# Optimization experiments

Hardware: AMD Instinct MI355X
Metric: run time of the kernel (lower is better)

## Reference

```python
import jax, jax.numpy as jnp
import numpy as np
from jax import lax

VOCAB = 10000
HID = 512
BATCH = 128
SEQ = 64
SCALE = 0.1


def setup_inputs() -> dict:
    key = jax.random.key(0)
    ks = jax.random.split(key, 16)
    u = lambda k, shape: jax.random.uniform(k, shape, jnp.float32, -SCALE, SCALE)
    return {
        "features": jax.random.randint(ks[0], (BATCH, SEQ), 0, VOCAB, jnp.int32),
        "labels": jax.random.randint(ks[1], (BATCH, SEQ), 0, VOCAB, jnp.int32),
        "seq_lengths": jax.random.randint(ks[2], (BATCH,), 0, SEQ, jnp.int32),
        "seq_mask": jax.random.uniform(ks[3], (BATCH, SEQ), jnp.float32),
        "embedding": u(ks[4], (VOCAB, HID)),
        "W0x": u(ks[5], (HID, 4 * HID)),
        "W0h": u(ks[6], (HID, 4 * HID)),
        "b0": jnp.zeros((4 * HID,), jnp.float32),
        "W1x": u(ks[7], (HID, 4 * HID)),
        "W1h": u(ks[8], (HID, 4 * HID)),
        "b1": jnp.zeros((4 * HID,), jnp.float32),
        "softmax_w": u(ks[9], (HID, VOCAB)),
        "softmax_b": jnp.zeros((VOCAB,), jnp.float32),
    }


def _lstm_cell(h, c, xin, Wx, Wh, b, m):
    # forget_bias = 0.0 (as in LSTMBlockCell(forget_bias=0.0))
    g = xin @ Wx + h @ Wh + b            # [B, 4H]
    i, cg, f, o = jnp.split(g, 4, axis=-1)
    c_new = jax.nn.sigmoid(f) * c + jax.nn.sigmoid(i) * jnp.tanh(cg)
    h_new = jax.nn.sigmoid(o) * jnp.tanh(c_new)
    # sequence_length masking: freeze state, zero output past length
    return m * h_new + (1 - m) * h, m * c_new + (1 - m) * c, m * h_new


def reference(features, labels, seq_lengths, seq_mask, embedding,
              W0x, W0h, b0, W1x, W1h, b1, softmax_w, softmax_b):
    x = embedding[features]                       # [B, T, H]
    B, T, H = x.shape
    xs = jnp.swapaxes(x, 0, 1)                    # [T, B, H]
    act = (jnp.arange(T)[:, None] < seq_lengths[None, :]).astype(x.dtype)[..., None]  # [T,B,1]

    def step(carry, inp):
        h0, c0, h1, c1 = carry
        xt, m = inp
        h0, c0, o0 = _lstm_cell(h0, c0, xt, W0x, W0h, b0, m)
        h1, c1, o1 = _lstm_cell(h1, c1, o0, W1x, W1h, b1, m)
        return (h0, c0, h1, c1), o1

    init = tuple(jnp.zeros((B, H), x.dtype) for _ in range(4))
    _, outs = lax.scan(step, init, (xs, act))     # [T, B, H]
    out = jnp.swapaxes(outs, 0, 1)                # [B, T, H]

    logits = out @ softmax_w + softmax_b          # [B, T, V]
    logp = jax.nn.log_softmax(logits, axis=-1)
    xent = -jnp.take_along_axis(logp, labels[..., None], axis=-1)[..., 0]  # [B, T]
    # tf.contrib.seq2seq.sequence_loss(average_across_batch=True, average_across_timesteps=False)
    loss_t = jnp.sum(xent * seq_mask, axis=0) / (jnp.sum(seq_mask, axis=0) + 1e-12)  # [T]
    cost = jnp.mean(loss_t)
    return cost
```

## Files before the change

### kernel.cpp

```cpp
#include <hip/hip_runtime.h>
#include <hip/hip_bf16.h>

#define BB 128
#define TT 64
#define HH 512
#define VV 10000
#define VP 10048
#define NTILES 157
#define NCHUNK 16
#define TPC 10
#define NBLK 256

typedef __attribute__((ext_vector_type(8))) __bf16 bf16x8;
typedef __attribute__((ext_vector_type(4))) float f32x4;
typedef unsigned short ushort_t;

__device__ __forceinline__ ushort_t f2bf(float x) {
  union { float f; unsigned u; } v; v.f = x;
  unsigned r = v.u + 0x7fffu + ((v.u >> 16) & 1u);
  return (ushort_t)(r >> 16);
}

__device__ __forceinline__ f32x4 mfma16(bf16x8 a, bf16x8 b, f32x4 c) {
  return __builtin_amdgcn_mfma_f32_16x16x32_bf16(a, b, c, 0, 0, 0);
}

__device__ __forceinline__ bf16x8 load16_sc1(const ushort_t* p) {
  bf16x8 r;
  asm volatile("global_load_dwordx4 %0, %1, off sc1" : "=v"(r) : "v"(p) : "memory");
  return r;
}

__device__ __forceinline__ void store16B_sc1(ushort_t* p, bf16x8 v) {
  asm volatile("global_store_dwordx4 %0, %1, off sc1" :: "v"(p), "v"(v) : "memory");
}

__device__ __forceinline__ void group_barrier(unsigned* bar, unsigned target, int grp) {
  asm volatile("s_waitcnt vmcnt(0)" ::: "memory");
  __syncthreads();
  if (threadIdx.x == 0) {
    const unsigned old = __hip_atomic_fetch_add(&bar[grp * 16], 1u,
                                                __ATOMIC_RELAXED, __HIP_MEMORY_SCOPE_AGENT);
    if (old + 1 == 64u * target)
      __hip_atomic_store(&bar[256 + grp * 16], target, __ATOMIC_RELAXED,
                         __HIP_MEMORY_SCOPE_AGENT);
    while (__hip_atomic_load(&bar[256 + grp * 16], __ATOMIC_RELAXED,
                             __HIP_MEMORY_SCOPE_AGENT) < target)
      __builtin_amdgcn_s_sleep(1);
  }
  __syncthreads();
}

__global__ void k_trans_w(const float* __restrict__ Wx0, const float* __restrict__ Wh0,
                          const float* __restrict__ Wx1, const float* __restrict__ Wh1,
                          ushort_t* __restrict__ dst0, ushort_t* __restrict__ dst1) {
  __shared__ float tile[64][65];
  const int kt = blockIdx.x * 64;
  const int ct = blockIdx.y * 64;
  const float* Wx = blockIdx.z ? Wx1 : Wx0;
  const float* Wh = blockIdx.z ? Wh1 : Wh0;
  ushort_t* dst = blockIdx.z ? dst1 : dst0;
  const int tid = threadIdx.x;
  const int cl = tid & 63;
  const int cp = ct + cl;
  const int col = (cp & 3) * 512 + (cp >> 2);
#pragma unroll
  for (int r = 0; r < 16; ++r) {
    const int kl = r * 4 + (tid >> 6);
    const int k = kt + kl;
    tile[cl][kl] = (k < 512) ? Wx[k * 2048 + col] : Wh[(k - 512) * 2048 + col];
  }
  __syncthreads();
#pragma unroll
  for (int s = 0; s < 16; ++s) {
    const int idx = tid + s * 256;
    const int cl2 = idx >> 6, kl2 = idx & 63;
    dst[(size_t)(ct + cl2) * 1024 + kt + kl2] = f2bf(tile[cl2][kl2]);
  }
}

__global__ void k_trans_sw(const float* __restrict__ sw, ushort_t* __restrict__ dst) {
  __shared__ float tile[64][65];
  const int kt = blockIdx.x * 64;
  const int vt = blockIdx.y * 64;
  const int tid = threadIdx.x;
  const int vl = tid & 63;
  const int v = vt + vl;
#pragma unroll
  for (int r = 0; r < 16; ++r) {
    const int kl = r * 4 + (tid >> 6);
    tile[vl][kl] = (v < VV) ? sw[(size_t)(kt + kl) * VV + v] : 0.f;
  }
  __syncthreads();
#pragma unroll
  for (int s = 0; s < 16; ++s) {
    const int idx = tid + s * 256;
    const int vl2 = idx >> 6, kl2 = idx & 63;
    dst[(size_t)(vt + vl2) * 512 + kt + kl2] = f2bf(tile[vl2][kl2]);
  }
}

__global__ void k_misc(const int* __restrict__ feat, const float* __restrict__ emb,
                       ushort_t* __restrict__ xb, ushort_t* __restrict__ h0,
                       ushort_t* __restrict__ h1, unsigned* __restrict__ bar) {
  const int stride = gridDim.x * blockDim.x;
  for (int e = blockIdx.x * blockDim.x + threadIdx.x; e < 8192 * 512; e += stride) {
    const int row = e >> 9;
    const int t = row >> 7, b = row & 127;
    const int f = feat[b * 64 + t];
    xb[e] = f2bf(emb[(size_t)f * 512 + (e & 511)]);
    if (e < 2 * 128 * 512) { h0[e] = 0; h1[e] = 0; }
    if (e < 512) bar[e] = 0u;
  }
}

__global__ __launch_bounds__(256, 1) void k_scan(
    const ushort_t* __restrict__ xb, const ushort_t* __restrict__ W0t,
    const ushort_t* __restrict__ W1t, const float* __restrict__ b0,
    const float* __restrict__ b1, ushort_t* __restrict__ h0g,
    ushort_t* __restrict__ h1g, ushort_t* __restrict__ out1,
    const int* __restrict__ seqlen, unsigned* __restrict__ bar) {
  __shared__ ushort_t act[32 * 128 * 8];
  __shared__ ushort_t hst[32][16];
  __shared__ ushort_t ost[32][16];
  __shared__ int sl_sh[32];
  const int bid = blockIdx.x;
  const int layer = bid >> 7;
  const int lb = bid & 127;
  const int cblk = lb >> 2;
  const int bquad = lb & 3;
  const int grp = bid & 3;
  const int tid = threadIdx.x;
  const int w = tid >> 6;
  const int lane = tid & 63;
  const int fr = lane & 15;
  const int hi = lane >> 4;
  const int w4hi = w * 4 + hi;

  const ushort_t* Wt = layer ? W1t : W0t;
  const float* bias = layer ? b1 : b0;
  ushort_t* hbuf = layer ? h1g : h0g;

  if (tid < 32) sl_sh[tid] = seqlen[bquad * 32 + tid];

  bf16x8 wreg[32];
  {
    const ushort_t* wp = Wt + (size_t)(cblk * 64 + w * 16 + fr) * 1024 + hi * 8;
#pragma unroll
    for (int ks = 0; ks < 32; ++ks)
      wreg[ks] = *reinterpret_cast<const bf16x8*>(wp + ks * 32);
  }

  const int u = cblk * 16 + w4hi;
  const float bi = bias[u];
  const float bc = bias[512 + u];
  const float bf_ = bias[1024 + u];
  const float bo = bias[1536 + u];

  __syncthreads();
  const int sl0 = sl_sh[fr];
  const int sl1 = sl_sh[fr + 16];

  float c0s = 0.f, c1s = 0.f;
  float h0s = 0.f, h1s = 0.f;

#pragma unroll 1
  for (int p = 0; p <= 64; ++p) {
    const int t = layer ? (p - 1) : p;
    const bool active = layer ? (p >= 1) : (p < 64);

    if (layer == 0 && active) {
      const ushort_t* xsrc = xb + (size_t)t * 128 * 512;
#pragma unroll
      for (int i = 0; i < 8; ++i) {
        const int idx = i * 256 + tid;
        const int b = idx >> 6;
        const int kp = idx & 63;
        const int kslot = (kp & 0x30) | ((kp & 15) ^ (b & 15));
        const ushort_t* s = xsrc + (size_t)(bquad * 32 + b) * 512 + (kslot << 3);
        *reinterpret_cast<bf16x8*>(&act[(b * 128 + kp) * 8]) =
            *reinterpret_cast<const bf16x8*>(s);
      }
    }

    group_barrier(bar, (unsigned)(p + 1), grp);

    if (active) {
      if (layer == 1) {
        bf16x8 tmp[16];
        const ushort_t* xsrc = h0g + (size_t)(p & 1) * 128 * 512;
        const ushort_t* hsrc = h1g + (size_t)(t & 1) * 128 * 512;
        int dsts[16];
#pragma unroll
        for (int i = 0; i < 8; ++i) {
          const int idx = i * 256 + tid;
          const int b = idx >> 6;
          const int kp = idx & 63;
          const int kslot = (kp & 0x30) | ((kp & 15) ^ (b & 15));
          tmp[i] = load16_sc1(xsrc + (size_t)(bquad * 32 + b) * 512 + (kslot << 3));
          dsts[i] = (b * 128 + kp) * 8;
        }
#pragma unroll
        for (int i = 0; i < 8; ++i) {
          const int idx = i * 256 + tid;
          const int b = idx >> 6;
          const int kp = 64 + (idx & 63);
          const int kslot = (kp & 0x70) | ((kp & 15) ^ (b & 15));
          tmp[8 + i] = load16_sc1(hsrc + (size_t)(bquad * 32 + b) * 512 + ((kslot - 64) << 3));
          dsts[8 + i] = (b * 128 + kp) * 8;
        }
        asm volatile("s_waitcnt vmcnt(0)" ::: "memory");
        __builtin_amdgcn_sched_barrier(0);
        const bf16x8 ZV = {};
#pragma unroll
        for (int i = 0; i < 8; ++i) {
          const int b = (i * 256 + tid) >> 6;
          *reinterpret_cast<bf16x8*>(&act[dsts[i]]) = (t < sl_sh[b]) ? tmp[i] : ZV;
        }
#pragma unroll
        for (int i = 0; i < 8; ++i)
          *reinterpret_cast<bf16x8*>(&act[dsts[8 + i]]) = tmp[8 + i];
      } else {
        bf16x8 tmp[8];
        const ushort_t* hsrc = h0g + (size_t)(t & 1) * 128 * 512;
        int dsts[8];
#pragma unroll
        for (int i = 0; i < 8; ++i) {
          const int idx = i * 256 + tid;
          const int b = idx >> 6;
          const int kp = 64 + (idx & 63);
          const int kslot = (kp & 0x70) | ((kp & 15) ^ (b & 15));
          tmp[i] = load16_sc1(hsrc + (size_t)(bquad * 32 + b) * 512 + ((kslot - 64) << 3));
          dsts[i] = (b * 128 + kp) * 8;
        }
        asm volatile("s_waitcnt vmcnt(0)" ::: "memory");
        __builtin_amdgcn_sched_barrier(0);
#pragma unroll
        for (int i = 0; i < 8; ++i)
          *reinterpret_cast<bf16x8*>(&act[dsts[i]]) = tmp[i];
      }
      __syncthreads();

      f32x4 acc0 = (f32x4){0.f, 0.f, 0.f, 0.f};
      f32x4 acc1 = (f32x4){0.f, 0.f, 0.f, 0.f};
#pragma unroll
      for (int ks = 0; ks < 32; ++ks) {
        const int kslot = ks * 4 + hi;
        const int kp = (kslot & 0x70) | ((kslot & 15) ^ fr);
        const bf16x8 bf0 = *reinterpret_cast<const bf16x8*>(&act[(fr * 128 + kp) * 8]);
        const bf16x8 bf1 = *reinterpret_cast<const bf16x8*>(&act[((16 + fr) * 128 + kp) * 8]);
        acc0 = mfma16(wreg[ks], bf0, acc0);
        acc1 = mfma16(wreg[ks], bf1, acc1);
      }
      __syncthreads();

      {
        const float si = 1.f / (1.f + __expf(-(acc0[0] + bi)));
        const float tc = tanhf(acc0[1] + bc);
        const float sf = 1.f / (1.f + __expf(-(acc0[2] + bf_)));
        const float so = 1.f / (1.f + __expf(-(acc0[3] + bo)));
        const float cn = sf * c0s + si * tc;
        const float hn = so * tanhf(cn);
        const bool msk = t < sl0;
        if (msk) { c0s = cn; h0s = hn; }
        hst[fr][w4hi] = f2bf(h0s);
        if (layer) ost[fr][w4hi] = msk ? f2bf(hn) : (ushort_t)0;
      }
      {
        const float si = 1.f / (1.f + __expf(-(acc1[0] + bi)));
        const float tc = tanhf(acc1[1] + bc);
        const float sf = 1.f / (1.f + __expf(-(acc1[2] + bf_)));
        const float so = 1.f / (1.f + __expf(-(acc1[3] + bo)));
        const float cn = sf * c1s + si * tc;
        const float hn = so * tanhf(cn);
        const bool msk = t < sl1;
        if (msk) { c1s = cn; h1s = hn; }
        hst[fr + 16][w4hi] = f2bf(h1s);
        if (layer) ost[fr + 16][w4hi] = msk ? f2bf(hn) : (ushort_t)0;
      }
      __syncthreads();

      if (tid < 64) {
        const int bl = tid >> 1, hf = tid & 1;
        const size_t off = (size_t)(bquad * 32 + bl) * 512 + cblk * 16 + hf * 8;
        ushort_t* hp = hbuf + (size_t)((t + 1) & 1) * 128 * 512 + off;
        const bf16x8 hv = *reinterpret_cast<const bf16x8*>(&hst[bl][hf * 8]);
        store16B_sc1(hp, hv);
        if (layer) {
          const bf16x8 ovv = *reinterpret_cast<const bf16x8*>(&ost[bl][hf * 8]);
          *reinterpret_cast<bf16x8*>(out1 + (size_t)t * 128 * 512 + off) = ovv;
        }
      }
    }
  }
}

__global__ __launch_bounds__(256, 2) void k_loss_gemm(
    const ushort_t* __restrict__ A, const ushort_t* __restrict__ SWT,
    const float* __restrict__ sb, const int* __restrict__ labels,
    float* __restrict__ part) {
  __shared__ ushort_t Bl[64 * 512];
  const int tid = threadIdx.x;
  const int lane = tid & 63;
  const int w = tid >> 6;
  const int fr = lane & 15;
  const int fk = (lane >> 4) << 3;
  const int rowbase = blockIdx.x * 128 + w * 32;
  const int chunk = blockIdx.y;
  const int tile_lo = chunk * TPC;
  const int tile_hi = (tile_lo + TPC < NTILES) ? (tile_lo + TPC) : NTILES;

  bf16x8 a[2][16];
#pragma unroll
  for (int rf = 0; rf < 2; ++rf) {
    const ushort_t* ap = A + (size_t)(rowbase + rf * 16 + fr) * 512 + fk;
#pragma unroll
    for (int ks = 0; ks < 16; ++ks) a[rf][ks] = *reinterpret_cast<const bf16x8*>(ap + ks * 32);
  }

  int lab[2][4];
  float m[2][4], l[2][4], ll[2][4];
#pragma unroll
  for (int rf = 0; rf < 2; ++rf)
#pragma unroll
    for (int r = 0; r < 4; ++r) {
      const int rg = rowbase + rf * 16 + ((lane >> 4) << 2) + r;
      lab[rf][r] = labels[(rg & 127) * 64 + (rg >> 7)];
      m[rf][r] = -3.0e38f; l[rf][r] = 0.f; ll[rf][r] = 0.f;
    }

  for (int tile = tile_lo; tile < tile_hi; ++tile) {
    const ushort_t* bsrc = SWT + (size_t)tile * 64 * 512;
    __syncthreads();
#pragma unroll
    for (int s = 0; s < 16; ++s) {
      const int h = (s * 256 + tid) << 3;
      const int v = h >> 9;
      const int kb = (h & 511) >> 3;
      *reinterpret_cast<bf16x8*>(&Bl[v * 512 + ((kb ^ (v & 7)) << 3)]) =
          *reinterpret_cast<const bf16x8*>(bsrc + h);
    }
    __syncthreads();

    f32x4 acc[2][4];
#pragma unroll
    for (int rf = 0; rf < 2; ++rf)
#pragma unroll
      for (int cf = 0; cf < 4; ++cf) acc[rf][cf] = (f32x4){0.f, 0.f, 0.f, 0.f};

#pragma unroll
    for (int ks = 0; ks < 16; ++ks) {
#pragma unroll
      for (int cf = 0; cf < 4; ++cf) {
        const int v = cf * 16 + fr;
        const int kb = (ks * 32 + fk) >> 3;
        const bf16x8 b =
            *reinterpret_cast<const bf16x8*>(&Bl[v * 512 + ((kb ^ (v & 7)) << 3)]);
        acc[0][cf] = mfma16(a[0][ks], b, acc[0][cf]);
        acc[1][cf] = mfma16(a[1][ks], b, acc[1][cf]);
      }
    }

    const int vb = tile * 64;
    float sbt[4]; bool vld[4];
#pragma unroll
    for (int cf = 0; cf < 4; ++cf) {
      const int v = vb + cf * 16 + fr;
      vld[cf] = v < VV;
      sbt[cf] = vld[cf] ? sb[v] : 0.f;
    }
#pragma unroll
    for (int rf = 0; rf < 2; ++rf)
#pragma unroll
      for (int r = 0; r < 4; ++r) {
        const float x0 = vld[0] ? acc[rf][0][r] + sbt[0] : -3.0e38f;
        const float x1 = vld[1] ? acc[rf][1][r] + sbt[1] : -3.0e38f;
        const float x2 = vld[2] ? acc[rf][2][r] + sbt[2] : -3.0e38f;
        const float x3 = vld[3] ? acc[rf][3][r] + sbt[3] : -3.0e38f;
        const float tm = fmaxf(fmaxf(x0, x1), fmaxf(x2, x3));
        if (tm > -1.0e37f) {
          const float mn = fmaxf(m[rf][r], tm);
          const float sc = __expf(m[rf][r] - mn);
          const float se = __expf(x0 - mn) + __expf(x1 - mn) +
                           __expf(x2 - mn) + __expf(x3 - mn);
          l[rf][r] = l[rf][r] * sc + se;
          m[rf][r] = mn;
        }
        const int lt = lab[rf][r] - vb;
        if (lt >= 0 && lt < 64 && fr == (lt & 15)) {
          const int cf = lt >> 4;
          ll[rf][r] += (cf == 0) ? x0 : (cf == 1) ? x1 : (cf == 2) ? x2 : x3;
        }
      }
  }

#pragma unroll
  for (int rf = 0; rf < 2; ++rf)
#pragma unroll
    for (int r = 0; r < 4; ++r) {
      float mm = m[rf][r], lv = l[rf][r], lv2 = ll[rf][r];
#pragma unroll
      for (int sh = 1; sh < 16; sh <<= 1) {
        const float m2 = __shfl_xor(mm, sh, 64);
        const float l2 = __shfl_xor(lv, sh, 64);
        const float ll2 = __shfl_xor(lv2, sh, 64);
        const float mn = fmaxf(mm, m2);
        lv = lv * __expf(mm - mn) + l2 * __expf(m2 - mn);
        mm = mn;
        lv2 += ll2;
      }
      if (fr == 0) {
        const int rg = rowbase + rf * 16 + ((lane >> 4) << 2) + r;
        float* p = part + ((size_t)chunk * 8192 + rg) * 4;
        p[0] = mm; p[1] = lv; p[2] = lv2;
      }
    }
}

__global__ void k_loss_merge(const float* __restrict__ part, float* __restrict__ xent) {
  const int row = blockIdx.x * 256 + threadIdx.x;
  float m = -3.0e38f, l = 0.f, ll = 0.f;
#pragma unroll
  for (int c = 0; c < NCHUNK; ++c) {
    const float* p = part + ((size_t)c * 8192 + row) * 4;
    const float pm = p[0], pl = p[1], pll = p[2];
    const float mn = fmaxf(m, pm);
    l = l * __expf(m - mn) + pl * __expf(pm - mn);
    m = mn;
    ll += pll;
  }
  xent[row] = m + logf(l) - ll;
}

__global__ void k_final(const float* __restrict__ xent, const float* __restrict__ mask,
                        float* __restrict__ out) {
  __shared__ float partial[4];
  const int lane = threadIdx.x & 63;
  const int w = threadIdx.x >> 6;
  float accT = 0.f;
  for (int i = 0; i < 16; ++i) {
    const int t = w * 16 + i;
    const float m1 = mask[lane * 64 + t];
    const float m2 = mask[(lane + 64) * 64 + t];
    float s = xent[t * 128 + lane] * m1 + xent[t * 128 + lane + 64] * m2;
    float sm = m1 + m2;
#pragma unroll
    for (int sh = 1; sh < 64; sh <<= 1) {
      s += __shfl_xor(s, sh, 64);
      sm += __shfl_xor(sm, sh, 64);
    }
    accT += s / (sm + 1e-12f);
  }
  if (lane == 0) partial[w] = accT;
  __syncthreads();
  if (threadIdx.x == 0)
    out[0] = (partial[0] + partial[1] + partial[2] + partial[3]) * (1.f / 64.f);
}

extern "C" void kernel_launch(void* const* d_in, const int* in_sizes, int n_in,
                              void* d_out, int out_size, void* d_ws, size_t ws_size,
                              hipStream_t stream) {
  const int* feat = (const int*)d_in[0];
  const int* labels = (const int*)d_in[1];
  const int* seqlen = (const int*)d_in[2];
  const float* seqmask = (const float*)d_in[3];
  const float* emb = (const float*)d_in[4];
  const float* W0x = (const float*)d_in[5];
  const float* W0h = (const float*)d_in[6];
  const float* b0 = (const float*)d_in[7];
  const float* W1x = (const float*)d_in[8];
  const float* W1h = (const float*)d_in[9];
  const float* b1 = (const float*)d_in[10];
  const float* sw = (const float*)d_in[11];
  const float* sbv = (const float*)d_in[12];

  ushort_t* W0t = (ushort_t*)d_ws;
  ushort_t* W1t = W0t + (size_t)2048 * 1024;
  ushort_t* SWT = W1t + (size_t)2048 * 1024;
  ushort_t* xb = SWT + (size_t)VP * 512;
  ushort_t* out1 = xb + (size_t)8192 * 512;
  ushort_t* h0g = out1 + (size_t)8192 * 512;
  ushort_t* h1g = h0g + (size_t)2 * 128 * 512;
  float* xent = (float*)(h1g + (size_t)2 * 128 * 512);
  float* part = xent + 8192;
  unsigned* bar = (unsigned*)(part + (size_t)NCHUNK * 8192 * 4);

  k_trans_w<<<dim3(16, 32, 2), 256, 0, stream>>>(W0x, W0h, W1x, W1h, W0t, W1t);
  k_trans_sw<<<dim3(8, 157), 256, 0, stream>>>(sw, SWT);
  k_misc<<<4096, 256, 0, stream>>>(feat, emb, xb, h0g, h1g, bar);

  {
    const ushort_t* a0 = xb; const ushort_t* a1 = W0t; const ushort_t* a2 = W1t;
    const float* a3 = b0; const float* a4 = b1;
    ushort_t* a5 = h0g; ushort_t* a6 = h1g; ushort_t* a7 = out1;
    const int* a8 = seqlen; unsigned* a9 = bar;
    void* args[] = {(void*)&a0, (void*)&a1, (void*)&a2, (void*)&a3, (void*)&a4,
                    (void*)&a5, (void*)&a6, (void*)&a7, (void*)&a8, (void*)&a9};
    hipLaunchCooperativeKernel((const void*)k_scan, dim3(NBLK), dim3(256), args, 0, stream);
  }

  k_loss_gemm<<<dim3(64, NCHUNK), 256, 0, stream>>>(out1, SWT, sbv, labels, part);
  k_loss_merge<<<32, 256, 0, stream>>>(part, xent);
  k_final<<<1, 256, 0, stream>>>(xent, seqmask, (float*)d_out);
}
```

Measured before the change: 547.1 us.

## Double-buffer loss GEMM with direct global-to-LDS loads, split scan barrier, fast gates

The loss GEMM now stages half-tiles of the pre-swizzled softmax weights straight into double-buffered LDS with global_load_lds. The next half-tile loads while the current one is computed, and the softmax bias is cached in shared memory. The softmax-weight transpose kernel writes the XOR-swizzled layout directly, so the staging copy needs no per-element remap. In the scan, the group barrier is split so the arrive happens before the layer-0 input prefetch and the wait after it, and sigmoid/tanh use exp plus a hardware reciprocal. This targets load latency in the loss GEMM and barrier idle time in the scan, at some cost in activation precision.

```diff
diff --git a/kernel.cpp b/kernel.cpp
--- a/kernel.cpp
+++ b/kernel.cpp
@@ -25,6 +25,13 @@
   return __builtin_amdgcn_mfma_f32_16x16x32_bf16(a, b, c, 0, 0, 0);
 }
 
+__device__ __forceinline__ float fsig(float x) {
+  return __builtin_amdgcn_rcpf(1.f + __expf(-x));
+}
+__device__ __forceinline__ float ftanh(float x) {
+  return 1.f - 2.f * __builtin_amdgcn_rcpf(__expf(2.f * x) + 1.f);
+}
+
 __device__ __forceinline__ bf16x8 load16_sc1(const ushort_t* p) {
   bf16x8 r;
   asm volatile("global_load_dwordx4 %0, %1, off sc1" : "=v"(r) : "v"(p) : "memory");
@@ -35,20 +42,10 @@
   asm volatile("global_store_dwordx4 %0, %1, off sc1" :: "v"(p), "v"(v) : "memory");
 }
 
-__device__ __forceinline__ void group_barrier(unsigned* bar, unsigned target, int grp) {
-  asm volatile("s_waitcnt vmcnt(0)" ::: "memory");
-  __syncthreads();
-  if (threadIdx.x == 0) {
-    const unsigned old = __hip_atomic_fetch_add(&bar[grp * 16], 1u,
-                                                __ATOMIC_RELAXED, __HIP_MEMORY_SCOPE_AGENT);
-    if (old + 1 == 64u * target)
-      __hip_atomic_store(&bar[256 + grp * 16], target, __ATOMIC_RELAXED,
-                         __HIP_MEMORY_SCOPE_AGENT);
-    while (__hip_atomic_load(&bar[256 + grp * 16], __ATOMIC_RELAXED,
-                             __HIP_MEMORY_SCOPE_AGENT) < target)
-      __builtin_amdgcn_s_sleep(1);
-  }
-  __syncthreads();
+__device__ __forceinline__ void glds16(const ushort_t* g, ushort_t* l) {
+  __builtin_amdgcn_global_load_lds(
+      (const __attribute__((address_space(1))) unsigned*)g,
+      (__attribute__((address_space(3))) unsigned*)l, 16, 0, 0);
 }
 
 __global__ void k_trans_w(const float* __restrict__ Wx0, const float* __restrict__ Wh0,
@@ -96,7 +93,10 @@
   for (int s = 0; s < 16; ++s) {
     const int idx = tid + s * 256;
     const int vl2 = idx >> 6, kl2 = idx & 63;
-    dst[(size_t)(vt + vl2) * 512 + kt + kl2] = f2bf(tile[vl2][kl2]);
+    const int k = kt + kl2;
+    const int kb = k >> 3;
+    const int kp = (((kb ^ (vl2 & 7)) << 3) | (k & 7));
+    dst[(size_t)(vt + vl2) * 512 + kp] = f2bf(tile[vl2][kl2]);
   }
 }
 
@@ -169,6 +169,15 @@
     const int t = layer ? (p - 1) : p;
     const bool active = layer ? (p >= 1) : (p < 64);
 
+    asm volatile("s_waitcnt vmcnt(0)" ::: "memory");
+    __syncthreads();
+    if (tid == 0) {
+      const unsigned old = __hip_atomic_fetch_add(&bar[grp * 16], 1u,
+                                                  __ATOMIC_RELAXED, __HIP_MEMORY_SCOPE_AGENT);
+      if (old + 1 == 64u * (unsigned)(p + 1))
+        __hip_atomic_store(&bar[256 + grp * 16], (unsigned)(p + 1), __ATOMIC_RELAXED,
+                           __HIP_MEMORY_SCOPE_AGENT);
+    }
     if (layer == 0 && active) {
       const ushort_t* xsrc = xb + (size_t)t * 128 * 512;
 #pragma unroll
@@ -182,8 +191,12 @@
             *reinterpret_cast<const bf16x8*>(s);
       }
     }
-
-    group_barrier(bar, (unsigned)(p + 1), grp);
+    if (tid == 0) {
+      while (__hip_atomic_load(&bar[256 + grp * 16], __ATOMIC_RELAXED,
+                               __HIP_MEMORY_SCOPE_AGENT) < (unsigned)(p + 1))
+        __builtin_amdgcn_s_sleep(1);
+    }
+    __syncthreads();
 
     if (active) {
       if (layer == 1) {
@@ -255,24 +268,24 @@
       __syncthreads();
 
       {
-        const float si = 1.f / (1.f + __expf(-(acc0[0] + bi)));
-        const float tc = tanhf(acc0[1] + bc);
-        const float sf = 1.f / (1.f + __expf(-(acc0[2] + bf_)));
-        const float so = 1.f / (1.f + __expf(-(acc0[3] + bo)));
+        const float si = fsig(acc0[0] + bi);
+        const float tc = ftanh(acc0[1] + bc);
+        const float sf = fsig(acc0[2] + bf_);
+        const float so = fsig(acc0[3] + bo);
         const float cn = sf * c0s + si * tc;
-        const float hn = so * tanhf(cn);
+        const float hn = so * ftanh(cn);
         const bool msk = t < sl0;
         if (msk) { c0s = cn; h0s = hn; }
         hst[fr][w4hi] = f2bf(h0s);
         if (layer) ost[fr][w4hi] = msk ? f2bf(hn) : (ushort_t)0;
       }
       {
-        const float si = 1.f / (1.f + __expf(-(acc1[0] + bi)));
-        const float tc = tanhf(acc1[1] + bc);
-        const float sf = 1.f / (1.f + __expf(-(acc1[2] + bf_)));
-        const float so = 1.f / (1.f + __expf(-(acc1[3] + bo)));
+        const float si = fsig(acc1[0] + bi);
+        const float tc = ftanh(acc1[1] + bc);
+        const float sf = fsig(acc1[2] + bf_);
+        const float so = fsig(acc1[3] + bo);
         const float cn = sf * c1s + si * tc;
-        const float hn = so * tanhf(cn);
+        const float hn = so * ftanh(cn);
         const bool msk = t < sl1;
         if (msk) { c1s = cn; h1s = hn; }
         hst[fr + 16][w4hi] = f2bf(h1s);
@@ -296,10 +309,11 @@
 }
 
 __global__ __launch_bounds__(256, 2) void k_loss_gemm(
-    const ushort_t* __restrict__ A, const ushort_t* __restrict__ SWT,
+    const ushort_t* __restrict__ A, const ushort_t* __restrict__ SWTs,
     const float* __restrict__ sb, const int* __restrict__ labels,
     float* __restrict__ part) {
-  __shared__ ushort_t Bl[64 * 512];
+  __shared__ ushort_t Bl[2][32 * 512];
+  __shared__ float sbl[640];
   const int tid = threadIdx.x;
   const int lane = tid & 63;
   const int w = tid >> 6;
@@ -309,6 +323,12 @@
   const int chunk = blockIdx.y;
   const int tile_lo = chunk * TPC;
   const int tile_hi = (tile_lo + TPC < NTILES) ? (tile_lo + TPC) : NTILES;
+  const int nhalf = (tile_hi - tile_lo) * 2;
+
+  for (int i = tid; i < 640; i += 256) {
+    const int v = chunk * 640 + i;
+    sbl[i] = (v < VV) ? sb[v] : 0.f;
+  }
 
   bf16x8 a[2][16];
 #pragma unroll
@@ -328,71 +348,100 @@
       lab[rf][r] = labels[(rg & 127) * 64 + (rg >> 7)];
       m[rf][r] = -3.0e38f; l[rf][r] = 0.f; ll[rf][r] = 0.f;
     }
-
-  for (int tile = tile_lo; tile < tile_hi; ++tile) {
-    const ushort_t* bsrc = SWT + (size_t)tile * 64 * 512;
-    __syncthreads();
-#pragma unroll
-    for (int s = 0; s < 16; ++s) {
-      const int h = (s * 256 + tid) << 3;
-      const int v = h >> 9;
-      const int kb = (h & 511) >> 3;
-      *reinterpret_cast<bf16x8*>(&Bl[v * 512 + ((kb ^ (v & 7)) << 3)]) =
-          *reinterpret_cast<const bf16x8*>(bsrc + h);
-    }
-    __syncthreads();
-
-    f32x4 acc[2][4];
-#pragma unroll
-    for (int rf = 0; rf < 2; ++rf)
-#pragma unroll
-      for (int cf = 0; cf < 4; ++cf) acc[rf][cf] = (f32x4){0.f, 0.f, 0.f, 0.f};
-
-#pragma unroll
-    for (int ks = 0; ks < 16; ++ks) {
+  __syncthreads();
+
+#define STAGE(BUF, HIDX)                                                         \
+  do {                                                                           \
+    const size_t gbase = (size_t)(tile_lo * 2 + (HIDX)) * 32 * 512;              \
+    _Pragma("unroll")                                                            \
+    for (int i_ = 0; i_ < 8; ++i_) {                                             \
+      glds16(SWTs + gbase + (size_t)(i_ * 256 + tid) * 8,                        \
+             &Bl[BUF][i_ * 2048 + w * 512]);                                     \
+    }                                                                            \
+  } while (0)
+
+  f32x4 acc[2][4];
+  STAGE(0, 0);
+
+#pragma unroll 1
+  for (int idx = 0; idx < nhalf; ++idx) {
+    const int cur = idx & 1;
+    if (idx + 1 < nhalf) {
+      STAGE(cur ^ 1, idx + 1);
+      asm volatile("s_waitcnt vmcnt(8)" ::: "memory");
+    } else {
+      asm volatile("s_waitcnt vmcnt(0)" ::: "memory");
+    }
+    __builtin_amdgcn_s_barrier();
+    __builtin_amdgcn_sched_barrier(0);
+
+    if ((idx & 1) == 0) {
+      acc[0][0] = (f32x4){0.f,0.f,0.f,0.f}; acc[0][1] = (f32x4){0.f,0.f,0.f,0.f};
+      acc[1][0] = (f32x4){0.f,0.f,0.f,0.f}; acc[1][1] = (f32x4){0.f,0.f,0.f,0.f};
+#pragma unroll
+      for (int ks = 0; ks < 16; ++ks) {
+#pragma unroll
+        for (int j = 0; j < 2; ++j) {
+          const int vloc = j * 16 + fr;
+          const int kb = ks * 4 + (fk >> 3);
+          const bf16x8 b = *reinterpret_cast<const bf16x8*>(
+              &Bl[cur][vloc * 512 + ((kb ^ (vloc & 7)) << 3)]);
+          acc[0][j] = mfma16(a[0][ks], b, acc[0][j]);
+          acc[1][j] = mfma16(a[1][ks], b, acc[1][j]);
+        }
+      }
+    } else {
+      acc[0][2] = (f32x4){0.f,0.f,0.f,0.f}; acc[0][3] = (f32x4){0.f,0.f,0.f,0.f};
+      acc[1][2] = (f32x4){0.f,0.f,0.f,0.f}; acc[1][3] = (f32x4){0.f,0.f,0.f,0.f};
+#pragma unroll
+      for (int ks = 0; ks < 16; ++ks) {
+#pragma unroll
+        for (int j = 0; j < 2; ++j) {
+          const int vloc = j * 16 + fr;
+          const int kb = ks * 4 + (fk >> 3);
+          const bf16x8 b = *reinterpret_cast<const bf16x8*>(
+              &Bl[cur][vloc * 512 + ((kb ^ (vloc & 7)) << 3)]);
+          acc[0][2 + j] = mfma16(a[0][ks], b, acc[0][2 + j]);
+          acc[1][2 + j] = mfma16(a[1][ks], b, acc[1][2 + j]);
+        }
+      }
+
+      const int tl = idx >> 1;
+      const int vb = (tile_lo + tl) * 64;
+      float sbt[4]; bool vld[4];
 #pragma unroll
       for (int cf = 0; cf < 4; ++cf) {
-        const int v = cf * 16 + fr;
-        const int kb = (ks * 32 + fk) >> 3;
-        const bf16x8 b =
-            *reinterpret_cast<const bf16x8*>(&Bl[v * 512 + ((kb ^ (v & 7)) << 3)]);
-        acc[0][cf] = mfma16(a[0][ks], b, acc[0][cf]);
-        acc[1][cf] = mfma16(a[1][ks], b, acc[1][cf]);
-      }
-    }
-
-    const int vb = tile * 64;
-    float sbt[4]; bool vld[4];
-#pragma unroll
-    for (int cf = 0; cf < 4; ++cf) {
-      const int v = vb + cf * 16 + fr;
-      vld[cf] = v < VV;
-      sbt[cf] = vld[cf] ? sb[v] : 0.f;
-    }
-#pragma unroll
-    for (int rf = 0; rf < 2; ++rf)
-#pragma unroll
-      for (int r = 0; r < 4; ++r) {
-        const float x0 = vld[0] ? acc[rf][0][r] + sbt[0] : -3.0e38f;
-        const float x1 = vld[1] ? acc[rf][1][r] + sbt[1] : -3.0e38f;
-        const float x2 = vld[2] ? acc[rf][2][r] + sbt[2] : -3.0e38f;
-        const float x3 = vld[3] ? acc[rf][3][r] + sbt[3] : -3.0e38f;
-        const float tm = fmaxf(fmaxf(x0, x1), fmaxf(x2, x3));
-        if (tm > -1.0e37f) {
-          const float mn = fmaxf(m[rf][r], tm);
-          const float sc = __expf(m[rf][r] - mn);
-          const float se = __expf(x0 - mn) + __expf(x1 - mn) +
-                           __expf(x2 - mn) + __expf(x3 - mn);
-          l[rf][r] = l[rf][r] * sc + se;
-          m[rf][r] = mn;
-        }
-        const int lt = lab[rf][r] - vb;
-        if (lt >= 0 && lt < 64 && fr == (lt & 15)) {
-          const int cf = lt >> 4;
-          ll[rf][r] += (cf == 0) ? x0 : (cf == 1) ? x1 : (cf == 2) ? x2 : x3;
-        }
-      }
-  }
+        const int v = vb + cf * 16 + fr;
+        vld[cf] = v < VV;
+        sbt[cf] = sbl[tl * 64 + cf * 16 + fr];
+      }
+#pragma unroll
+      for (int rf = 0; rf < 2; ++rf)
+#pragma unroll
+        for (int r = 0; r < 4; ++r) {
+          const float x0 = vld[0] ? acc[rf][0][r] + sbt[0] : -3.0e38f;
+          const float x1 = vld[1] ? acc[rf][1][r] + sbt[1] : -3.0e38f;
+          const float x2 = vld[2] ? acc[rf][2][r] + sbt[2] : -3.0e38f;
+          const float x3 = vld[3] ? acc[rf][3][r] + sbt[3] : -3.0e38f;
+          const float tm = fmaxf(fmaxf(x0, x1), fmaxf(x2, x3));
+          if (tm > -1.0e37f) {
+            const float mn = fmaxf(m[rf][r], tm);
+            const float sc = __expf(m[rf][r] - mn);
+            const float se = __expf(x0 - mn) + __expf(x1 - mn) +
+                             __expf(x2 - mn) + __expf(x3 - mn);
+            l[rf][r] = l[rf][r] * sc + se;
+            m[rf][r] = mn;
+          }
+          const int lt = lab[rf][r] - vb;
+          if (lt >= 0 && lt < 64 && fr == (lt & 15)) {
+            const int cf = lt >> 4;
+            ll[rf][r] += (cf == 0) ? x0 : (cf == 1) ? x1 : (cf == 2) ? x2 : x3;
+          }
+        }
+    }
+    __builtin_amdgcn_s_barrier();
+  }
+#undef STAGE
 
 #pragma unroll
   for (int rf = 0; rf < 2; ++rf)
```

Measured after the change: 475.1 us (median of 3 runs). 1.15x faster.
